# Performance work log

Hardware: AMD Instinct MI355X
Metric: run time of the kernel (lower is better)

Reference implementation:

```python
import jax, jax.numpy as jnp
import numpy as np
import math

B, S, V, D = 512, 256, 100000, 64
KS = [7, 5]
NF = [8, 16]
K_TOP = 4
NCLS = 6
ROWS = [D, D // 2, D // 4]  # [64, 32, 16]


def setup_inputs() -> dict:
    key = jax.random.key(0)
    ks = jax.random.split(key, 6)
    x = jax.random.randint(ks[0], (B, S), 0, V)
    emb = jax.random.normal(ks[1], (V, D), jnp.float32) * 0.1
    # conv1: in=1*64, out=8*64=512, groups=64 -> weight (512, 1, 7)
    w1 = jax.random.normal(ks[2], (NF[0] * ROWS[0], 1, KS[0]), jnp.float32) * 0.1
    b1 = jnp.zeros((NF[0] * ROWS[0],), jnp.float32)
    # conv2: in=8*32=256, out=16*32=512, groups=32 -> weight (512, 8, 5)
    w2 = jax.random.normal(ks[3], (NF[1] * ROWS[1], NF[0], KS[1]), jnp.float32) * 0.05
    b2 = jnp.zeros((NF[1] * ROWS[1],), jnp.float32)
    fc_in = ROWS[2] * NF[1] * K_TOP  # 16*16*4 = 1024
    fc_w = jax.random.normal(ks[4], (NCLS, fc_in), jnp.float32) * 0.05
    fc_b = jnp.zeros((NCLS,), jnp.float32)
    return dict(x=x, emb=emb, w1=w1, b1=b1, w2=w2, b2=b2, fc_w=fc_w, fc_b=fc_b)


def _kmax_ordered(h, k):
    # order-preserving k-max pooling along last axis
    _, idx = jax.lax.top_k(h, k)
    idx = jnp.sort(idx, axis=-1)
    return jnp.take_along_axis(h, idx, axis=-1)


def _forward(x, emb, w1, b1, w2, b2, fc_w, fc_b):
    h = emb[x].transpose(0, 2, 1)  # (B, D, S)
    ws, bs = (w1, w2), (b1, b2)
    L = len(KS)
    for i in range(L):
        K = KS[i]
        nf = NF[i]
        groups = ROWS[i]
        # wide grouped conv1d, padding = K-1 both sides -> out_len = S + K - 1
        h = jax.lax.conv_general_dilated(
            h, ws[i], window_strides=(1,), padding=[(K - 1, K - 1)],
            dimension_numbers=('NCH', 'OIH', 'NCH'), feature_group_count=groups,
        ) + bs[i][None, :, None]
        b_, d_, s_ = h.shape
        # to_channel_view: (b, d, s) -> (b, nf, d//nf, s)
        h = h.reshape(b_, d_ // nf, nf, s_).transpose(0, 2, 1, 3)
        # Fold(2,2): sum adjacent row pairs along the row axis
        h = h.reshape(b_, nf, (d_ // nf) // 2, 2, s_).sum(axis=3)
        # from_channel_view: (b, nf, rows, s) -> (b, rows*nf, s)
        h = h.transpose(0, 2, 1, 3).reshape(b_, -1, s_)
        # dynamic k-max pool (last layer uses fixed k_top)
        if i == L - 1:
            k = K_TOP
        else:
            k = max(K_TOP, math.ceil((L - (i + 1)) / L * h.shape[-1]))
        h = _kmax_ordered(h, k)
        h = jnp.tanh(h)
    # dropout is identity in eval mode
    h = h.reshape(h.shape[0], -1)  # (B, rows[-1]*nf[-1]*k_top) = (B, 1024)
    return h @ fc_w.T + fc_b


def reference(x, emb, w1, b1, w2, b2, fc_w, fc_b):
    return _forward(x, emb, w1, b1, w2, b2, fc_w, fc_b)
```

## Files before the change

kernel.cpp:

```cpp
#include <hip/hip_runtime.h>
#include <stdint.h>

#define S_LEN 256
#define OUT1  262
#define K1SEL 131
#define OUT2  135
#define W1T_OFF 0
#define W2T_OFF 3584
#define B1C_OFF 24064
#define B2C_OFF 24320
#define WREG    1120

typedef float v2f __attribute__((ext_vector_type(2)));
__device__ __forceinline__ v2f fma2(v2f a, v2f b, v2f c) {
    return __builtin_elementwise_fma(a, b, c);
}

__device__ __forceinline__ int lane_prefix(unsigned long long m) {
    return __builtin_amdgcn_mbcnt_hi((uint32_t)(m >> 32),
           __builtin_amdgcn_mbcnt_lo((uint32_t)m, 0));
}
__device__ __forceinline__ uint32_t f2ord(float x) {
    uint32_t b = __float_as_uint(x);
    return (b & 0x80000000u) ? ~b : (b | 0x80000000u);
}
__device__ __forceinline__ float ord2f(uint32_t s) {
    uint32_t b = (s & 0x80000000u) ? (s & 0x7FFFFFFFu) : ~s;
    return __uint_as_float(b);
}
__device__ __forceinline__ float fast_tanh(float x) {
    float e = __expf(2.0f * x);
    return (e - 1.0f) * __builtin_amdgcn_rcpf(e + 1.0f);
}
typedef unsigned long long u64;
__device__ __forceinline__ u64 shflx64(u64 v, int m) {
    uint32_t lo = (uint32_t)__shfl_xor((int)(uint32_t)v, m, 64);
    uint32_t hi = (uint32_t)__shfl_xor((int)(uint32_t)(v >> 32), m, 64);
    return ((u64)hi << 32) | lo;
}
__device__ __forceinline__ u64 maxu64(u64 a, u64 b) { return a > b ? a : b; }
__device__ __forceinline__ u64 minu64(u64 a, u64 b) { return a < b ? a : b; }

extern "C" __global__ void dcnn_prep(const float* __restrict__ w1, const float* __restrict__ b1,
                                     const float* __restrict__ w2, const float* __restrict__ b2,
                                     const float* __restrict__ fcb, float* __restrict__ out,
                                     float* __restrict__ ws) {
    int i = blockIdx.x * 256 + threadIdx.x;
    if (i < 3072) out[i] = fcb[i % 6];
    if (i < W2T_OFF) {
        int d = i / 56, r = i % 56, k = r / 8, f = r % 8;
        ws[i] = w1[(d * 8 + f) * 7 + k];
    } else if (i < B1C_OFF) {
        int q = i - W2T_OFF;
        int g = q / 640, r = q % 640;
        int ic = r / 80, r2 = r % 80;
        int k = r2 / 16, f2 = r2 % 16;
        ws[i] = w2[((g * 16 + f2) * 8 + ic) * 5 + k];
    } else if (i < B2C_OFF) {
        int q = i - B1C_OFF;
        int r2 = q / 8, f = q % 8;
        ws[i] = b1[(2 * r2) * 8 + f] + b1[(2 * r2 + 1) * 8 + f];
    } else {
        int q = i - B2C_OFF;
        int r3 = q / 16, f2 = q % 16;
        ws[i] = b2[(2 * r3) * 16 + f2] + b2[(2 * r3 + 1) * 16 + f2];
    }
}

extern "C" __global__
__attribute__((amdgpu_flat_work_group_size(256, 256), amdgpu_waves_per_eu(4, 8)))
void dcnn_main(const int* __restrict__ x, const float* __restrict__ emb,
               const float* __restrict__ fcw, const float* __restrict__ ws,
               float* __restrict__ out) {
    __shared__ float uni[4 * WREG];
    __shared__ int   xs[S_LEN];
    __shared__ float p2loc[128];
    __shared__ float fred[2][6];

    const int tid    = threadIdx.x;
    const int lane   = tid & 63;
    const int wv     = __builtin_amdgcn_readfirstlane(tid >> 6);
    const int sample = blockIdx.x >> 3;
    const int q8     = blockIdx.x & 7;
    const int sl     = q8 * 2 + (wv >> 1);
    const int rs     = wv & 1;

    const float* w1t = ws + W1T_OFF;
    const float* w2t = ws + W2T_OFF;
    const float* b1c = ws + B1C_OFF;
    const float* b2c = ws + B2C_OFF;

    xs[tid] = x[sample * S_LEN + tid];
    __syncthreads();

    float*  reg   = uni + wv * WREG;
    float2* rowsW = (float2*)reg;
    float*  p1w   = reg;

    if (lane < 8) {
        rowsW[lane]       = make_float2(0.f, 0.f);
        rowsW[264 + lane] = make_float2(0.f, 0.f);
    }
    const int dbase = 4 * sl + 2 * rs;
#pragma unroll
    for (int m = 0; m < 4; ++m) {
        int j  = lane + 64 * m;
        int xi = xs[j];
        rowsW[8 + j] = *(const float2*)(emb + (size_t)xi * 64 + dbase);
    }

    v2f acc2[4][5];
#pragma unroll
    for (int j = 0; j < 4; ++j) {
        v2f bz = *(const v2f*)(b1c + (2 * sl + rs) * 8 + 2 * j);
#pragma unroll
        for (int m = 0; m < 5; ++m) acc2[j][m] = bz;
    }
    int tA[5];
#pragma unroll
    for (int m = 0; m < 5; ++m) { int t = lane + 64 * m; tA[m] = (t < OUT1) ? t : (OUT1 - 1); }

#pragma unroll 1
    for (int k = 0; k < 7; ++k) {
        v2f wa[4], wb[4];
#pragma unroll
        for (int j = 0; j < 4; ++j) {
            wa[j] = *(const v2f*)(w1t + (dbase * 7 + k) * 8 + 2 * j);
            wb[j] = *(const v2f*)(w1t + ((dbase + 1) * 7 + k) * 8 + 2 * j);
        }
#pragma unroll
        for (int m = 0; m < 5; ++m) {
            float2 v = rowsW[tA[m] + 2 + k];
            v2f vx = { v.x, v.x };
            v2f vy = { v.y, v.y };
#pragma unroll
            for (int j = 0; j < 4; ++j) {
                acc2[j][m] = fma2(wa[j], vx, acc2[j][m]);
                acc2[j][m] = fma2(wb[j], vy, acc2[j][m]);
            }
        }
    }

    {
        int c = lane >> 3, j = lane & 7;
        int pos = (j < 4) ? j : (131 + j);
        p1w[c * 140 + pos] = 0.f;
    }

#pragma unroll
    for (int cp = 0; cp < 4; ++cp) {
        uint32_t uA[5], uB[5];
#pragma unroll
        for (int m = 0; m < 5; ++m) {
            int t = lane + 64 * m;
            uA[m] = (t < OUT1) ? f2ord(acc2[cp][m].x) : 0u;
            uB[m] = (t < OUT1) ? f2ord(acc2[cp][m].y) : 0u;
        }
        uint32_t preA = 0, preB = 0;
#pragma unroll 1
        for (int bit = 31; bit >= 16; --bit) {
            uint32_t cA = preA | (1u << bit);
            uint32_t cB = preB | (1u << bit);
            int na = 0, nb = 0;
#pragma unroll
            for (int m = 0; m < 5; ++m) {
                na += __popcll(__ballot(uA[m] >= cA));
                nb += __popcll(__ballot(uB[m] >= cB));
            }
            if (na >= K1SEL) preA = cA;
            if (nb >= K1SEL) preB = cB;
        }
        int gA = 0, gB = 0, eA = 0, eB = 0;
        uint32_t pA16 = preA >> 16, pB16 = preB >> 16;
#pragma unroll
        for (int m = 0; m < 5; ++m) {
            gA += __popcll(__ballot((uA[m] >> 16) >  pA16));
            eA += __popcll(__ballot((uA[m] >> 16) == pA16));
            gB += __popcll(__ballot((uB[m] >> 16) >  pB16));
            eB += __popcll(__ballot((uB[m] >> 16) == pB16));
        }
        uint32_t msk = 0xFFFF0000u;
        int cgtA, cgtB;
        if ((K1SEL - gA < eA) || (K1SEL - gB < eB)) {
#pragma unroll 1
            for (int bit = 15; bit >= 0; --bit) {
                uint32_t cA = preA | (1u << bit);
                uint32_t cB = preB | (1u << bit);
                int na = 0, nb = 0;
#pragma unroll
                for (int m = 0; m < 5; ++m) {
                    na += __popcll(__ballot(uA[m] >= cA));
                    nb += __popcll(__ballot(uB[m] >= cB));
                }
                if (na >= K1SEL) preA = cA;
                if (nb >= K1SEL) preB = cB;
            }
            msk = 0xFFFFFFFFu;
            cgtA = 0; cgtB = 0;
#pragma unroll
            for (int m = 0; m < 5; ++m) {
                cgtA += __popcll(__ballot(uA[m] > preA));
                cgtB += __popcll(__ballot(uB[m] > preB));
            }
        } else {
            cgtA = gA; cgtB = gB;
        }
        const int needA = K1SEL - cgtA;
        const int needB = K1SEL - cgtB;
        float* dstA = p1w + (2 * cp) * 140 + 4;
        float* dstB = p1w + (2 * cp + 1) * 140 + 4;
        int eqA = 0, kpA = 0, eqB = 0, kpB = 0;
#pragma unroll
        for (int m = 0; m < 5; ++m) {
            uint32_t umA = uA[m] & msk;
            uint32_t umB = uB[m] & msk;
            unsigned long long emA = __ballot(umA == preA);
            unsigned long long emB = __ballot(umB == preB);
            int erA = eqA + lane_prefix(emA);
            int erB = eqB + lane_prefix(emB);
            bool keepA = (umA > preA) || ((umA == preA) && (erA < needA));
            bool keepB = (umB > preB) || ((umB == preB) && (erB < needB));
            unsigned long long kmA = __ballot(keepA);
            unsigned long long kmB = __ballot(keepB);
            int posA = kpA + lane_prefix(kmA);
            int posB = kpB + lane_prefix(kmB);
            if (keepA) dstA[posA] = ord2f(uA[m]);
            if (keepB) dstB[posB] = ord2f(uB[m]);
            eqA += __popcll(emA); kpA += __popcll(kmA);
            eqB += __popcll(emB); kpB += __popcll(kmB);
        }
    }

#pragma unroll
    for (int i = 0; i < 17; ++i) {
        int idx = lane + 64 * i;
        p1w[idx] = fast_tanh(p1w[idx]);
    }
    if (lane < 32) {
        int idx = lane + 64 * 17;
        p1w[idx] = fast_tanh(p1w[idx]);
    }

    v2f a2v[8][3];
    {
        const v2f* b2v = (const v2f*)(b2c + sl * 16);
#pragma unroll
        for (int j = 0; j < 8; ++j) {
            v2f bz = rs ? (v2f){0.f, 0.f} : b2v[j];
            a2v[j][0] = bz; a2v[j][1] = bz; a2v[j][2] = bz;
        }
    }
    int tB[3];
#pragma unroll
    for (int tm = 0; tm < 3; ++tm) { int t = lane + 64 * tm; tB[tm] = (t < OUT2) ? t : (OUT2 - 1); }

    const int g = 2 * sl + rs;
#pragma unroll 1
    for (int ic = 0; ic < 8; ++ic) {
        const float* src = p1w + ic * 140;
        float win[3][5];
#pragma unroll
        for (int m = 0; m < 3; ++m) {
            win[m][0] = src[tB[m]];     win[m][1] = src[tB[m] + 1];
            win[m][2] = src[tB[m] + 2]; win[m][3] = src[tB[m] + 3];
            win[m][4] = src[tB[m] + 4];
        }
#pragma unroll
        for (int k = 0; k < 5; ++k) {
            const v2f* wv2 = (const v2f*)(w2t + ((g * 8 + ic) * 5 + k) * 16);
            v2f s0 = { win[0][k], win[0][k] };
            v2f s1 = { win[1][k], win[1][k] };
            v2f s2 = { win[2][k], win[2][k] };
#pragma unroll
            for (int j = 0; j < 8; ++j) {
                v2f w = wv2[j];
                a2v[j][0] = fma2(w, s0, a2v[j][0]);
                a2v[j][1] = fma2(w, s1, a2v[j][1]);
                a2v[j][2] = fma2(w, s2, a2v[j][2]);
            }
        }
    }

    float* scr = uni + (wv & ~1) * WREG;
    __syncthreads();
    if (rs) {
#pragma unroll
        for (int j = 0; j < 8; ++j) {
            scr[(2 * j) * 137 + lane]           = a2v[j][0].x;
            scr[(2 * j + 1) * 137 + lane]       = a2v[j][0].y;
            scr[(2 * j) * 137 + lane + 64]      = a2v[j][1].x;
            scr[(2 * j + 1) * 137 + lane + 64]  = a2v[j][1].y;
            if (lane + 128 < OUT2) {
                scr[(2 * j) * 137 + lane + 128]     = a2v[j][2].x;
                scr[(2 * j + 1) * 137 + lane + 128] = a2v[j][2].y;
            }
        }
    }
    __syncthreads();
    if (!rs) {
#pragma unroll
        for (int j = 0; j < 8; ++j) {
            scr[(2 * j) * 137 + lane]           += a2v[j][0].x;
            scr[(2 * j + 1) * 137 + lane]       += a2v[j][0].y;
            scr[(2 * j) * 137 + lane + 64]      += a2v[j][1].x;
            scr[(2 * j + 1) * 137 + lane + 64]  += a2v[j][1].y;
            if (lane + 128 < OUT2) {
                scr[(2 * j) * 137 + lane + 128]     += a2v[j][2].x;
                scr[(2 * j + 1) * 137 + lane + 128] += a2v[j][2].y;
            }
        }
    }
    __syncthreads();

    {
        const int f2o = (lane >> 3) + 8 * rs;
        const int seg = lane & 7;
        const int tstart = seg * 17;
        const int tend = (seg == 7) ? (OUT2 - 119) : 17;
        const float* src = scr + f2o * 137 + tstart;
        const uint32_t tb = 0xFFFFFFFFu - (uint32_t)tstart;
        u64 L0 = 0, L1 = 0, L2 = 0, L3 = 0;
#pragma unroll 1
        for (int i = 0; i < 17; ++i) {
            float v = src[(i < tend) ? i : 0];
            u64 kk = ((u64)f2ord(v) << 32) | (u64)(tb - (uint32_t)i);
            if (i >= tend) kk = 0;
            bool b0 = kk > L0, b1 = kk > L1, b2 = kk > L2, b3 = kk > L3;
            L3 = b3 ? (b2 ? L2 : kk) : L3;
            L2 = b2 ? (b1 ? L1 : kk) : L2;
            L1 = b1 ? (b0 ? L0 : kk) : L1;
            L0 = b0 ? kk : L0;
        }
#pragma unroll
        for (int d = 1; d <= 4; d <<= 1) {
            u64 M0 = shflx64(L0, d), M1 = shflx64(L1, d);
            u64 M2 = shflx64(L2, d), M3 = shflx64(L3, d);
            u64 r0 = maxu64(L0, M0);
            u64 r1 = minu64(maxu64(L0, M1), maxu64(L1, M0));
            u64 r2 = minu64(minu64(maxu64(L0, M2), maxu64(L1, M1)), maxu64(L2, M0));
            u64 r3k = minu64(minu64(maxu64(L0, M3), maxu64(L1, M2)),
                             minu64(maxu64(L2, M1), maxu64(L3, M0)));
            L0 = r0; L1 = r1; L2 = r2; L3 = r3k;
        }
        if (seg == 0) {
#define CSW2(a, bb) { if ((uint32_t)(bb) > (uint32_t)(a)) { u64 tt = (a); (a) = (bb); (bb) = tt; } }
            CSW2(L0, L1); CSW2(L2, L3); CSW2(L0, L2); CSW2(L1, L3); CSW2(L1, L2);
#undef CSW2
            float* qp = &p2loc[(wv >> 1) * 64 + f2o * 4];
            qp[0] = ord2f((uint32_t)(L0 >> 32));
            qp[1] = ord2f((uint32_t)(L1 >> 32));
            qp[2] = ord2f((uint32_t)(L2 >> 32));
            qp[3] = ord2f((uint32_t)(L3 >> 32));
        }
    }
    __syncthreads();

    if (wv < 2) {
        float pv = fast_tanh(p2loc[tid]);
        float part[6];
#pragma unroll
        for (int n = 0; n < 6; ++n) part[n] = pv * fcw[n * 1024 + q8 * 128 + tid];
#pragma unroll
        for (int n = 0; n < 6; ++n) {
            float s = part[n];
#pragma unroll
            for (int off = 32; off > 0; off >>= 1) s += __shfl_xor(s, off, 64);
            if (lane == 0) fred[wv][n] = s;
        }
    }
    __syncthreads();
    if (tid < 6)
        atomicAdd(&out[sample * 6 + tid], fred[0][tid] + fred[1][tid]);
}

extern "C" void kernel_launch(void* const* d_in, const int* in_sizes, int n_in,
                              void* d_out, int out_size, void* d_ws, size_t ws_size,
                              hipStream_t stream) {
    (void)in_sizes; (void)n_in; (void)out_size; (void)ws_size;
    const int*   x   = (const int*)d_in[0];
    const float* emb = (const float*)d_in[1];
    const float* w1  = (const float*)d_in[2];
    const float* b1  = (const float*)d_in[3];
    const float* w2  = (const float*)d_in[4];
    const float* b2  = (const float*)d_in[5];
    const float* fcw = (const float*)d_in[6];
    const float* fcb = (const float*)d_in[7];
    float* outp = (float*)d_out;
    float* wsf  = (float*)d_ws;

    dcnn_prep<<<96, 256, 0, stream>>>(w1, b1, w2, b2, fcb, outp, wsf);
    dcnn_main<<<4096, 256, 0, stream>>>(x, emb, fcw, wsf, outp);
}
```

Measured before the change: 218.9 us.

## Split work into 128-thread blocks, one slice per block

Each 256-thread block used to handle two slices of a sample across four waves. Now each 128-thread block handles one slice with two waves, so twice as many blocks are launched and each needs half the shared memory. The aim is finer-grained scheduling and higher occupancy, which could also cut barrier cost since fewer waves wait at each __syncthreads. The FC reduction now runs in a single wave and the atomics double to two per sample slice pair. The top-k masking is also simplified so the first four rows are always valid.

After: 222.1 us. No clear change (+1.5%).

```diff
diff --git a/kernel.cpp b/kernel.cpp
--- a/kernel.cpp
+++ b/kernel.cpp
@@ -68,29 +68,29 @@
 }
 
 extern "C" __global__
-__attribute__((amdgpu_flat_work_group_size(256, 256), amdgpu_waves_per_eu(4, 8)))
+__attribute__((amdgpu_flat_work_group_size(128, 128), amdgpu_waves_per_eu(4, 8)))
 void dcnn_main(const int* __restrict__ x, const float* __restrict__ emb,
                const float* __restrict__ fcw, const float* __restrict__ ws,
                float* __restrict__ out) {
-    __shared__ float uni[4 * WREG];
+    __shared__ float uni[2 * WREG];
     __shared__ int   xs[S_LEN];
-    __shared__ float p2loc[128];
-    __shared__ float fred[2][6];
+    __shared__ float p2loc[64];
+    __shared__ float fred6[6];
 
     const int tid    = threadIdx.x;
     const int lane   = tid & 63;
     const int wv     = __builtin_amdgcn_readfirstlane(tid >> 6);
-    const int sample = blockIdx.x >> 3;
-    const int q8     = blockIdx.x & 7;
-    const int sl     = q8 * 2 + (wv >> 1);
-    const int rs     = wv & 1;
+    const int sample = blockIdx.x >> 4;
+    const int sl     = blockIdx.x & 15;
+    const int rs     = wv;
 
     const float* w1t = ws + W1T_OFF;
     const float* w2t = ws + W2T_OFF;
     const float* b1c = ws + B1C_OFF;
     const float* b2c = ws + B2C_OFF;
 
-    xs[tid] = x[sample * S_LEN + tid];
+    xs[tid]       = x[sample * S_LEN + tid];
+    xs[tid + 128] = x[sample * S_LEN + tid + 128];
     __syncthreads();
 
     float*  reg   = uni + wv * WREG;
@@ -151,11 +151,12 @@
     for (int cp = 0; cp < 4; ++cp) {
         uint32_t uA[5], uB[5];
 #pragma unroll
-        for (int m = 0; m < 5; ++m) {
-            int t = lane + 64 * m;
-            uA[m] = (t < OUT1) ? f2ord(acc2[cp][m].x) : 0u;
-            uB[m] = (t < OUT1) ? f2ord(acc2[cp][m].y) : 0u;
-        }
+        for (int m = 0; m < 4; ++m) {
+            uA[m] = f2ord(acc2[cp][m].x);
+            uB[m] = f2ord(acc2[cp][m].y);
+        }
+        uA[4] = (lane < 6) ? f2ord(acc2[cp][4].x) : 0u;
+        uB[4] = (lane < 6) ? f2ord(acc2[cp][4].y) : 0u;
         uint32_t preA = 0, preB = 0;
 #pragma unroll 1
         for (int bit = 31; bit >= 16; --bit) {
@@ -281,7 +282,7 @@
         }
     }
 
-    float* scr = uni + (wv & ~1) * WREG;
+    float* scr = uni;
     __syncthreads();
     if (rs) {
 #pragma unroll
@@ -346,7 +347,7 @@
 #define CSW2(a, bb) { if ((uint32_t)(bb) > (uint32_t)(a)) { u64 tt = (a); (a) = (bb); (bb) = tt; } }
             CSW2(L0, L1); CSW2(L2, L3); CSW2(L0, L2); CSW2(L1, L3); CSW2(L1, L2);
 #undef CSW2
-            float* qp = &p2loc[(wv >> 1) * 64 + f2o * 4];
+            float* qp = &p2loc[f2o * 4];
             qp[0] = ord2f((uint32_t)(L0 >> 32));
             qp[1] = ord2f((uint32_t)(L1 >> 32));
             qp[2] = ord2f((uint32_t)(L2 >> 32));
@@ -355,22 +356,20 @@
     }
     __syncthreads();
 
-    if (wv < 2) {
-        float pv = fast_tanh(p2loc[tid]);
+    if (wv == 0) {
+        float pv = fast_tanh(p2loc[lane]);
         float part[6];
 #pragma unroll
-        for (int n = 0; n < 6; ++n) part[n] = pv * fcw[n * 1024 + q8 * 128 + tid];
+        for (int n = 0; n < 6; ++n) part[n] = pv * fcw[n * 1024 + sl * 64 + lane];
 #pragma unroll
         for (int n = 0; n < 6; ++n) {
             float s = part[n];
 #pragma unroll
             for (int off = 32; off > 0; off >>= 1) s += __shfl_xor(s, off, 64);
-            if (lane == 0) fred[wv][n] = s;
-        }
-    }
-    __syncthreads();
-    if (tid < 6)
-        atomicAdd(&out[sample * 6 + tid], fred[0][tid] + fred[1][tid]);
+            if (lane == 0) fred6[n] = s;
+        }
+        if (lane < 6) atomicAdd(&out[sample * 6 + lane], fred6[lane]);
+    }
 }
 
 extern "C" void kernel_launch(void* const* d_in, const int* in_sizes, int n_in,
@@ -389,5 +388,5 @@
     float* wsf  = (float*)d_ws;
 
     dcnn_prep<<<96, 256, 0, stream>>>(w1, b1, w2, b2, fcb, outp, wsf);
-    dcnn_main<<<4096, 256, 0, stream>>>(x, emb, fcw, wsf, outp);
-}
+    dcnn_main<<<8192, 128, 0, stream>>>(x, emb, fcw, wsf, outp);
+}
```
